# Kernel tuning notes

Hardware: AMD Instinct MI355X
Metric: run time of the kernel (lower is better)

## Reference

```python
import jax, jax.numpy as jnp
import numpy as np

D_MODEL = 1024
NUM_HEADS = 16
HEAD_DIM = D_MODEL // NUM_HEADS
HIDDEN = 4096
EPS = 1e-10


def _layernorm(x, gamma, beta):
    mean = jnp.mean(x, axis=-1, keepdims=True)
    var = jnp.var(x, axis=-1, keepdims=True)  # unbiased=False
    return gamma * (x - mean) / jnp.sqrt(var + EPS) + beta


def setup_inputs() -> dict:
    key = jax.random.key(0)
    ks = jax.random.split(key, 16)
    s = 0.02
    d, h = D_MODEL, HIDDEN
    inp = {
        "x": jax.random.normal(ks[0], (4, 2048, d), dtype=jnp.float32),
        "Wq": jax.random.normal(ks[1], (d, d), dtype=jnp.float32) * s,
        "bq": jnp.zeros((d,), jnp.float32),
        "Wk": jax.random.normal(ks[2], (d, d), dtype=jnp.float32) * s,
        "bk": jnp.zeros((d,), jnp.float32),
        "Wv": jax.random.normal(ks[3], (d, d), dtype=jnp.float32) * s,
        "bv": jnp.zeros((d,), jnp.float32),
        "Wo": jax.random.normal(ks[4], (d, d), dtype=jnp.float32) * s,
        "bo": jnp.zeros((d,), jnp.float32),
        "W1": jax.random.normal(ks[5], (d, h), dtype=jnp.float32) * s,
        "b1": jnp.zeros((h,), jnp.float32),
        "W2": jax.random.normal(ks[6], (h, d), dtype=jnp.float32) * s,
        "b2": jnp.zeros((d,), jnp.float32),
        "gamma1": jnp.ones((d,), jnp.float32),
        "beta1": jnp.zeros((d,), jnp.float32),
        "gamma2": jnp.ones((d,), jnp.float32),
        "beta2": jnp.zeros((d,), jnp.float32),
    }
    return inp


def reference(x, Wq, bq, Wk, bk, Wv, bv, Wo, bo, W1, b1, W2, b2,
              gamma1, beta1, gamma2, beta2):
    B, S, D = x.shape
    H, hd = NUM_HEADS, HEAD_DIM
    scale = jnp.sqrt(jnp.float32(hd))

    # --- sublayer 1: self-attention on norm(x), residual add ---
    xn = _layernorm(x, gamma1, beta1)
    Q = (xn @ Wq + bq).reshape(B, S, H, hd).transpose(0, 2, 1, 3)  # [B,H,S,hd]
    K = (xn @ Wk + bk).reshape(B, S, H, hd).transpose(0, 2, 1, 3)
    V = (xn @ Wv + bv).reshape(B, S, H, hd).transpose(0, 2, 1, 3)
    scores = jnp.einsum("bhqd,bhkd->bhqk", Q, K) / scale  # [B,H,S,S]
    attn = jax.nn.softmax(scores, axis=-1)
    ctx = jnp.einsum("bhqk,bhkd->bhqd", attn, V)  # [B,H,S,hd]
    ctx = ctx.transpose(0, 2, 1, 3).reshape(B, S, D)
    x = x + (ctx @ Wo + bo)

    # --- sublayer 2: FFN on norm(x), residual add ---
    xn = _layernorm(x, gamma2, beta2)
    h = jax.nn.gelu(xn @ W1 + b1, approximate=False)  # torch F.gelu default = erf
    x = x + (h @ W2 + b2)
    return x
```

## Files before the change

kernel.cpp:

```cpp
#include <hip/hip_runtime.h>
#include <stdint.h>

#define D_MODEL 1024
#define HIDDEN  4096
#define SEQ     2048
#define NTOK    8192
#define NHEAD   16
#define HDIM    64

typedef unsigned short u16;
typedef __attribute__((ext_vector_type(8))) __bf16 bf16x8;
typedef __attribute__((ext_vector_type(4))) float f32x4;

__device__ __forceinline__ u16 f2bf(float f) {
  union { float f; unsigned u; } c; c.f = f;
  unsigned u = c.u + 0x7fffu + ((c.u >> 16) & 1u);
  return (u16)(u >> 16);
}

__device__ __forceinline__ void gload16(const void* g, void* l) {
  __builtin_amdgcn_global_load_lds((const __attribute__((address_space(1))) void*)g,
                                   (__attribute__((address_space(3))) void*)l, 16, 0, 0);
}

__global__ void transpose_cvt4(const float* __restrict__ A0, const float* __restrict__ A1,
                               const float* __restrict__ A2, const float* __restrict__ A3,
                               u16* __restrict__ O) {
  __shared__ float t[32][33];
  const int z = blockIdx.z;
  const float* W = (z == 0) ? A0 : (z == 1) ? A1 : (z == 2) ? A2 : A3;
  u16* Wt = O + ((size_t)z << 20);
  const int k0 = blockIdx.y * 32, n0 = blockIdx.x * 32;
  const int tx = threadIdx.x, ty = threadIdx.y;
#pragma unroll
  for (int p = 0; p < 4; ++p)
    t[ty + p * 8][tx] = W[(size_t)(k0 + ty + p * 8) * D_MODEL + n0 + tx];
  __syncthreads();
#pragma unroll
  for (int p = 0; p < 4; ++p) {
    const int n = ty + p * 8;
    Wt[(size_t)(n0 + n) * D_MODEL + k0 + tx] = f2bf(t[tx][n]);
  }
}

__global__ void transpose_cvt(const float* __restrict__ W, u16* __restrict__ Wt, int K, int N) {
  __shared__ float t[32][33];
  const int k0 = blockIdx.y * 32, n0 = blockIdx.x * 32;
  const int tx = threadIdx.x, ty = threadIdx.y;
#pragma unroll
  for (int p = 0; p < 4; ++p)
    t[ty + p * 8][tx] = W[(size_t)(k0 + ty + p * 8) * N + n0 + tx];
  __syncthreads();
#pragma unroll
  for (int p = 0; p < 4; ++p) {
    const int n = ty + p * 8;
    Wt[(size_t)(n0 + n) * K + k0 + tx] = f2bf(t[tx][n]);
  }
}

__global__ __launch_bounds__(256)
void ln_kernel(const float* __restrict__ x, const float* __restrict__ gamma,
               const float* __restrict__ beta, u16* __restrict__ out) {
  const int row = blockIdx.x;
  const int tid = threadIdx.x;
  const float4 v = ((const float4*)(x + (size_t)row * D_MODEL))[tid];
  float s = v.x + v.y + v.z + v.w;
  float q = v.x * v.x + v.y * v.y + v.z * v.z + v.w * v.w;
#pragma unroll
  for (int o = 32; o > 0; o >>= 1) { s += __shfl_down(s, o); q += __shfl_down(q, o); }
  __shared__ float ps[4], pq[4];
  const int wid = tid >> 6, lane = tid & 63;
  if (lane == 0) { ps[wid] = s; pq[wid] = q; }
  __syncthreads();
  s = ps[0] + ps[1] + ps[2] + ps[3];
  q = pq[0] + pq[1] + pq[2] + pq[3];
  const float mean = s * (1.0f / D_MODEL);
  const float var = q * (1.0f / D_MODEL) - mean * mean;
  const float rstd = rsqrtf(var + 1e-10f);
  const float4 gv = ((const float4*)gamma)[tid];
  const float4 bv = ((const float4*)beta)[tid];
  ushort4 o4;
  o4.x = f2bf((v.x - mean) * rstd * gv.x + bv.x);
  o4.y = f2bf((v.y - mean) * rstd * gv.y + bv.y);
  o4.z = f2bf((v.z - mean) * rstd * gv.z + bv.z);
  o4.w = f2bf((v.w - mean) * rstd * gv.w + bv.w);
  ((ushort4*)(out + (size_t)row * D_MODEL))[tid] = o4;
}

template <int EPI, int KPY, int KPX>
__global__ __launch_bounds__(256, 3)
void gemm64(const u16* __restrict__ A, const u16* __restrict__ Bt,
            const float* __restrict__ bias, const float* __restrict__ bias2,
            const float* __restrict__ res, void* __restrict__ outp, void* __restrict__ outp2,
            int M, int N, int K) {
  __shared__ u16 As[128 * 64];
  __shared__ u16 Bs[128 * 64];
  const int tid = threadIdx.x;
  const int wid = tid >> 6, lane = tid & 63;
  const int g = lane >> 4, lr = lane & 15;
  const int wm = (wid & 1) << 6, wn = (wid >> 1) << 6;

  const int xcd = blockIdx.x & 7, l = blockIdx.x >> 3;
  int bx, by;
  if (KPY > 0) { by = xcd * KPY + (l % KPY); bx = l / KPY; }
  else         { bx = xcd * KPX + (l % KPX); by = l / KPX; }
  const int m0 = by * 128, n0 = bx * 128;

  const int NT = K >> 6;

  const int r0 = tid >> 3;
  const int csw = ((tid & 7) ^ (r0 & 7)) << 3;
  const u16* pA[4];
  const u16* pB[4];
#pragma unroll
  for (int i = 0; i < 4; ++i) {
    pA[i] = A + (size_t)(m0 + r0 + i * 32) * K + csw;
    pB[i] = Bt + (size_t)(n0 + r0 + i * 32) * K + csw;
  }
  const int db = (tid & 192) * 16;

  f32x4 acc[4][4] = {};

  for (int t = 0; t < NT; ++t) {
    __syncthreads();
#pragma unroll
    for (int i = 0; i < 4; ++i) {
      gload16(pA[i], (char*)As + db + i * 4096);
      gload16(pB[i], (char*)Bs + db + i * 4096);
      pA[i] += 64; pB[i] += 64;
    }
    __syncthreads();

#pragma unroll
    for (int ks = 0; ks < 2; ++ks) {
      bf16x8 af[4], bfr[4];
#pragma unroll
      for (int f = 0; f < 4; ++f) {
        const int ra = wm + f * 16 + lr;
        const int rb = wn + f * 16 + lr;
        const int co = ((ks * 4 + g) ^ (lr & 7)) * 8;
        af[f] = *(const bf16x8*)(As + ra * 64 + co);
        bfr[f] = *(const bf16x8*)(Bs + rb * 64 + co);
      }
      __builtin_amdgcn_s_setprio(1);
#pragma unroll
      for (int mf = 0; mf < 4; ++mf)
#pragma unroll
        for (int nf = 0; nf < 4; ++nf)
          acc[mf][nf] =
              __builtin_amdgcn_mfma_f32_16x16x32_bf16(af[mf], bfr[nf], acc[mf][nf], 0, 0, 0);
      __builtin_amdgcn_s_setprio(0);
    }
  }

#pragma unroll
  for (int mf = 0; mf < 4; ++mf)
#pragma unroll
    for (int nf = 0; nf < 4; ++nf) {
      const int gn = n0 + wn + nf * 16 + lr;
      const int gm = m0 + wm + mf * 16 + 4 * g;
#pragma unroll
      for (int r = 0; r < 4; ++r) {
        const float av = acc[mf][nf][r];
        if (EPI == 0) {
          ((u16*)outp)[(size_t)(gm + r) * N + gn] = f2bf(av + bias[gn]);
        } else if (EPI == 1) {
          const size_t idx = (size_t)(gm + r) * N + gn;
          ((float*)outp)[idx] = av + bias[gn] + res[idx];
        } else if (EPI == 2) {
          const float v = av + bias[gn];
          ((u16*)outp)[(size_t)(gm + r) * N + gn] =
              f2bf(0.5f * v * (1.0f + erff(v * 0.7071067811865475f)));
        } else if (EPI == 3) {
          const int gn_p = (gn & ~63) | ((gn & 15) << 2) | ((gn >> 4) & 3);
          ((u16*)outp)[(size_t)(gm + r) * N + gn_p] = f2bf(av + bias[gm + r]);
        } else {
          const int side = gn >> 10, col = gn & 1023;
          u16* o = (u16*)(side ? outp2 : outp);
          float t_ = av + (side ? bias2[col] : bias[col]);
          if (!side) t_ *= 0.18033688011112042f;
          o[(size_t)(gm + r) * 1024 + col] = f2bf(t_);
        }
      }
    }
}

__global__ __launch_bounds__(256, 4)
void attn_kernel(const u16* __restrict__ Q, const u16* __restrict__ K,
                 const u16* __restrict__ Vt, u16* __restrict__ ctxo) {
  const int L = blockIdx.x;
  const int q0 = ((L >> 3) & 15) * 128;
  const int bh = ((L >> 7) << 3) | (L & 7);
  const int b = bh >> 4, h = bh & 15;
  const int tid = threadIdx.x, wid = tid >> 6, lane = tid & 63;
  const int g = lane >> 4, lr = lane & 15;
  const size_t base = ((size_t)b * SEQ) * D_MODEL + h * HDIM;
  const size_t vbase = ((size_t)h * HDIM) * NTOK + (size_t)b * SEQ;

#define AST 76
  __shared__ u16 Ks[64 * AST];
  __shared__ u16 Vts[64 * AST];
  __shared__ u16 Ps[128 * AST];

  const int qw = wid * 32;

#pragma unroll
  for (int i = 0; i < 4; ++i) {
    const int ch = tid + 256 * i, row = ch >> 3, j = ch & 7;
    *(bf16x8*)(Ps + row * AST + j * 8) =
        *(const bf16x8*)(Q + base + (size_t)(q0 + row) * D_MODEL + j * 8);
  }
  __syncthreads();
  bf16x8 aq[2][2];
#pragma unroll
  for (int qf = 0; qf < 2; ++qf)
#pragma unroll
    for (int ks = 0; ks < 2; ++ks)
      aq[qf][ks] = *(const bf16x8*)(Ps + (qw + qf * 16 + lr) * AST + ks * 32 + g * 8);

  f32x4 o[2][4] = {};
  float lrun[2][4] = {};

  for (int kv0 = 0; kv0 < SEQ; kv0 += 64) {
    __syncthreads();
#pragma unroll
    for (int i = 0; i < 2; ++i) {
      const int row = (tid >> 3) + i * 32, j = tid & 7;
      *(bf16x8*)(Ks + row * AST + j * 8) =
          *(const bf16x8*)(K + base + (size_t)(kv0 + row) * D_MODEL + j * 8);
      *(bf16x8*)(Vts + row * AST + j * 8) =
          *(const bf16x8*)(Vt + vbase + (size_t)row * NTOK + kv0 + j * 8);
    }
    __syncthreads();

    f32x4 s[2][4] = {};
    __builtin_amdgcn_s_setprio(1);
#pragma unroll
    for (int ks = 0; ks < 2; ++ks)
#pragma unroll
      for (int kf = 0; kf < 4; ++kf) {
        const bf16x8 bk = *(const bf16x8*)(Ks + (kf * 16 + lr) * AST + ks * 32 + g * 8);
#pragma unroll
        for (int qf = 0; qf < 2; ++qf)
          s[qf][kf] = __builtin_amdgcn_mfma_f32_16x16x32_bf16(aq[qf][ks], bk, s[qf][kf], 0, 0, 0);
      }
    __builtin_amdgcn_s_setprio(0);

#pragma unroll
    for (int qf = 0; qf < 2; ++qf)
#pragma unroll
      for (int r = 0; r < 4; ++r) {
        float p0, p1, p2, p3;
        asm("v_exp_f32 %0, %1" : "=v"(p0) : "v"(s[qf][0][r]));
        asm("v_exp_f32 %0, %1" : "=v"(p1) : "v"(s[qf][1][r]));
        asm("v_exp_f32 %0, %1" : "=v"(p2) : "v"(s[qf][2][r]));
        asm("v_exp_f32 %0, %1" : "=v"(p3) : "v"(s[qf][3][r]));
        lrun[qf][r] += (p0 + p1) + (p2 + p3);
        unsigned lo, hi;
        asm("v_cvt_pk_bf16_f32 %0, %1, %2" : "=v"(lo) : "v"(p0), "v"(p1));
        asm("v_cvt_pk_bf16_f32 %0, %1, %2" : "=v"(hi) : "v"(p2), "v"(p3));
        *(uint2*)(Ps + (qw + qf * 16 + 4 * g + r) * AST + lr * 4) = make_uint2(lo, hi);
      }
    asm volatile("s_waitcnt lgkmcnt(0)" ::: "memory");

    __builtin_amdgcn_s_setprio(1);
#pragma unroll
    for (int ks = 0; ks < 2; ++ks) {
      bf16x8 pf[2];
#pragma unroll
      for (int qf = 0; qf < 2; ++qf)
        pf[qf] = *(const bf16x8*)(Ps + (qw + qf * 16 + lr) * AST + ks * 32 + g * 8);
#pragma unroll
      for (int df = 0; df < 4; ++df) {
        const bf16x8 vf = *(const bf16x8*)(Vts + (df * 16 + lr) * AST + ks * 32 + g * 8);
#pragma unroll
        for (int qf = 0; qf < 2; ++qf)
          o[qf][df] = __builtin_amdgcn_mfma_f32_16x16x32_bf16(pf[qf], vf, o[qf][df], 0, 0, 0);
      }
    }
    __builtin_amdgcn_s_setprio(0);
  }

#pragma unroll
  for (int off = 1; off < 16; off <<= 1)
#pragma unroll
    for (int qf = 0; qf < 2; ++qf)
#pragma unroll
      for (int r = 0; r < 4; ++r)
        lrun[qf][r] += __shfl_xor(lrun[qf][r], off);

#pragma unroll
  for (int qf = 0; qf < 2; ++qf)
#pragma unroll
    for (int r = 0; r < 4; ++r) {
      const float rinv = 1.0f / lrun[qf][r];
      const int qrow = q0 + qw + qf * 16 + 4 * g + r;
#pragma unroll
      for (int df = 0; df < 4; ++df)
        ctxo[base + (size_t)qrow * D_MODEL + df * 16 + lr] = f2bf(o[qf][df][r] * rinv);
    }
#undef AST
}

extern "C" void kernel_launch(void* const* d_in, const int* in_sizes, int n_in,
                              void* d_out, int out_size, void* d_ws, size_t ws_size,
                              hipStream_t stream) {
  const float* x  = (const float*)d_in[0];
  const float* Wq = (const float*)d_in[1];
  const float* bq = (const float*)d_in[2];
  const float* Wk = (const float*)d_in[3];
  const float* bk = (const float*)d_in[4];
  const float* Wv = (const float*)d_in[5];
  const float* bv = (const float*)d_in[6];
  const float* Wo = (const float*)d_in[7];
  const float* bo = (const float*)d_in[8];
  const float* W1 = (const float*)d_in[9];
  const float* b1 = (const float*)d_in[10];
  const float* W2 = (const float*)d_in[11];
  const float* b2 = (const float*)d_in[12];
  const float* gamma1 = (const float*)d_in[13];
  const float* beta1  = (const float*)d_in[14];
  const float* gamma2 = (const float*)d_in[15];
  const float* beta2  = (const float*)d_in[16];
  float* out = (float*)d_out;

  const size_t M1 = 1u << 20;
  u16* w   = (u16*)d_ws;
  u16* WtQ = w;
  u16* WtV = w + 2 * M1;
  u16* WtO = w + 3 * M1;
  u16* Wt1 = w + 4 * M1;
  u16* Wt2 = w + 8 * M1;
  u16* xn  = w + 12 * M1;
  u16* Qb  = w + 20 * M1;
  u16* Kb  = w + 28 * M1;
  u16* Vtb = w + 36 * M1;
  u16* ctx = w + 44 * M1;
  u16* hb  = w + 20 * M1;
  float* x1 = (float*)(w + 52 * M1);

  const dim3 tb(32, 8);
  transpose_cvt4<<<dim3(32, 32, 4), tb, 0, stream>>>(Wq, Wk, Wv, Wo, WtQ);
  transpose_cvt<<<dim3(HIDDEN / 32, D_MODEL / 32), tb, 0, stream>>>(W1, Wt1, D_MODEL, HIDDEN);
  transpose_cvt<<<dim3(D_MODEL / 32, HIDDEN / 32), tb, 0, stream>>>(W2, Wt2, HIDDEN, D_MODEL);

  ln_kernel<<<NTOK, 256, 0, stream>>>(x, gamma1, beta1, xn);

  gemm64<6, 8, 0><<<1024, 256, 0, stream>>>(xn, WtQ, bq, bk, nullptr, Qb, Kb,
                                            NTOK, 2048, D_MODEL);
  gemm64<3, 0, 8><<<512, 256, 0, stream>>>(WtV, xn, bv, nullptr, nullptr, Vtb, nullptr,
                                           D_MODEL, NTOK, D_MODEL);

  attn_kernel<<<1024, 256, 0, stream>>>(Qb, Kb, Vtb, ctx);

  gemm64<1, 8, 0><<<512, 256, 0, stream>>>(ctx, WtO, bo, nullptr, x, x1, nullptr,
                                           NTOK, D_MODEL, D_MODEL);

  ln_kernel<<<NTOK, 256, 0, stream>>>(x1, gamma2, beta2, xn);

  gemm64<2, 8, 0><<<2048, 256, 0, stream>>>(xn, Wt1, b1, nullptr, nullptr, hb, nullptr,
                                            NTOK, HIDDEN, D_MODEL);
  gemm64<1, 8, 0><<<512, 256, 0, stream>>>(hb, Wt2, b2, nullptr, x1, out, nullptr,
                                           NTOK, D_MODEL, HIDDEN);
}
```

Measured before the change: 353.3 us.

## Add 256x256 ping-pong pipelined GEMM kernel for FFN up-projection

Adds a new GEMM kernel with 256x256 output tiles, 512 threads and double-buffered LDS. It overlaps global-to-LDS loads with MFMA work through explicit vmcnt and barrier scheduling and raises MFMA priority with s_setprio. Only the FFN up-projection (W1 with GELU epilogue) uses it, replacing the smaller-tile gemm64. The goal is more operand reuse and better latency hiding, at the cost of one block per CU and heavy register and LDS use.

Result: slower. 366.0 us (+3.6%).

```diff
diff --git a/kernel.cpp b/kernel.cpp
--- a/kernel.cpp
+++ b/kernel.cpp
@@ -185,6 +185,138 @@
     }
 }
 
+template <int MH, int NH>
+__device__ __forceinline__ void mmq(f32x4 (&acc)[8][4], const bf16x8 (&av)[4][2],
+                                    const bf16x8 (&bv)[2][2]) {
+  __builtin_amdgcn_s_setprio(1);
+#pragma unroll
+  for (int f = 0; f < 4; ++f)
+#pragma unroll
+    for (int n = 0; n < 2; ++n)
+#pragma unroll
+      for (int ks = 0; ks < 2; ++ks)
+        acc[MH * 4 + f][NH * 2 + n] = __builtin_amdgcn_mfma_f32_16x16x32_bf16(
+            av[f][ks], bv[n][ks], acc[MH * 4 + f][NH * 2 + n], 0, 0, 0);
+  __builtin_amdgcn_s_setprio(0);
+}
+
+template <int EPI, int KPY, int KPX>
+__global__ __launch_bounds__(512, 1)
+void gemm256p(const u16* __restrict__ A, const u16* __restrict__ Bt,
+              const float* __restrict__ bias, const float* __restrict__ res,
+              void* __restrict__ outp, int M, int N, int K) {
+  __shared__ u16 Ls[65536];
+  const int tid = threadIdx.x;
+  const int wid = tid >> 6, lane = tid & 63;
+  const int g = lane >> 4, lr = lane & 15;
+  const int wm = wid >> 2, wn = wid & 3;
+
+  const int xcd = blockIdx.x & 7, l = blockIdx.x >> 3;
+  int bx, by;
+  if (KPY > 0) { by = xcd * KPY + (l % KPY); bx = l / KPY; }
+  else         { bx = xcd * KPX + (l % KPX); by = l / KPX; }
+  const int m0 = by * 256, n0 = bx * 256;
+
+  const int NT = K >> 6;
+
+  const int r0 = tid >> 3;
+  const int cc0 = ((tid & 7) ^ (r0 & 7)) << 3;
+  const u16* Abase = A + (size_t)(m0 + r0) * K + cc0;
+  const u16* Bbase = Bt + (size_t)(n0 + r0) * K + cc0;
+  const int dstb = wid << 10;
+
+  auto sA = [&](int d, int h, int tk) {
+    const u16* p = Abase + (size_t)(h * 128) * K + tk * 64;
+    char* q_ = (char*)Ls + d * 65536 + h * 16384 + dstb;
+    gload16(p, q_);
+    gload16(p + (size_t)64 * K, q_ + 8192);
+  };
+  auto sB = [&](int d, int h, int tk) {
+    const u16* p = Bbase + (size_t)(h * 128) * K + tk * 64;
+    char* q_ = (char*)Ls + d * 65536 + 32768 + h * 16384 + dstb;
+    gload16(p, q_);
+    gload16(p + (size_t)64 * K, q_ + 8192);
+  };
+
+  const int cof0 = ((g) ^ (lr & 7)) << 3;
+  const int cof1 = ((4 | g) ^ (lr & 7)) << 3;
+  const int aB = wm * 8192 + lr * 64;
+  const int bB = 16384 + (wn >> 1) * 8192 + (wn & 1) * 4096 + lr * 64;
+
+  f32x4 acc[8][4] = {};
+  bf16x8 a[4][2], a2[4][2], b[2][2], b2[2][2];
+
+  auto rdA = [&](bf16x8 (&dst)[4][2], int D, int mh) {
+#pragma unroll
+    for (int f = 0; f < 4; ++f) {
+      dst[f][0] = *(const bf16x8*)(Ls + D + aB + (mh * 4 + f) * 1024 + cof0);
+      dst[f][1] = *(const bf16x8*)(Ls + D + aB + (mh * 4 + f) * 1024 + cof1);
+    }
+  };
+  auto rdB = [&](bf16x8 (&dst)[2][2], int D, int nh) {
+#pragma unroll
+    for (int f = 0; f < 2; ++f) {
+      dst[f][0] = *(const bf16x8*)(Ls + D + bB + (nh * 2 + f) * 1024 + cof0);
+      dst[f][1] = *(const bf16x8*)(Ls + D + bB + (nh * 2 + f) * 1024 + cof1);
+    }
+  };
+
+#define BAR asm volatile("s_barrier" ::: "memory")
+#define LG0 asm volatile("s_waitcnt lgkmcnt(0)" ::: "memory")
+#define VM6 asm volatile("s_waitcnt vmcnt(6)" ::: "memory")
+#define VM0 asm volatile("s_waitcnt vmcnt(0)" ::: "memory")
+
+  sA(0, 0, 0); sA(0, 1, 0); sB(0, 0, 0); sB(0, 1, 0);
+  sA(1, 0, 1); sA(1, 1, 1); sB(1, 0, 1);
+  VM6;
+  BAR;
+
+  for (int T = 0; T < NT; T += 2) {
+    const bool s2 = (T + 2) < NT;
+    rdA(a, 0, 0); rdB(b, 0, 0); sB(1, 1, T + 1);
+    BAR; LG0; mmq<0, 0>(acc, a, b); BAR;
+    rdA(a2, 0, 1);
+    BAR; LG0; mmq<1, 0>(acc, a2, b); BAR;
+    rdB(b2, 0, 1); if (s2) sA(0, 0, T + 2);
+    BAR; LG0; mmq<1, 1>(acc, a2, b2); BAR;
+    if (s2) { sA(0, 1, T + 2); sB(0, 0, T + 2); VM6; } else VM0;
+    BAR; mmq<0, 1>(acc, a, b2); BAR;
+    rdA(a, 32768, 0); rdB(b, 32768, 0); if (s2) sB(0, 1, T + 2);
+    BAR; LG0; mmq<0, 0>(acc, a, b); BAR;
+    rdA(a2, 32768, 1);
+    BAR; LG0; mmq<1, 0>(acc, a2, b); BAR;
+    rdB(b2, 32768, 1); if (s2) sA(1, 0, T + 3);
+    BAR; LG0; mmq<1, 1>(acc, a2, b2); BAR;
+    if (s2) { sA(1, 1, T + 3); sB(1, 0, T + 3); VM6; } else VM0;
+    BAR; mmq<0, 1>(acc, a, b2); BAR;
+  }
+#undef BAR
+#undef LG0
+#undef VM6
+#undef VM0
+
+#pragma unroll
+  for (int mf = 0; mf < 8; ++mf)
+#pragma unroll
+    for (int nf = 0; nf < 4; ++nf) {
+      const int gn = n0 + wn * 64 + nf * 16 + lr;
+      const int gm = m0 + wm * 128 + mf * 16 + 4 * g;
+      const float bb = bias[gn];
+#pragma unroll
+      for (int r = 0; r < 4; ++r) {
+        const float av = acc[mf][nf][r];
+        if (EPI == 1) {
+          const size_t idx = (size_t)(gm + r) * N + gn;
+          ((float*)outp)[idx] = av + bb + res[idx];
+        } else {
+          const float v = av + bb;
+          ((u16*)outp)[(size_t)(gm + r) * N + gn] =
+              f2bf(0.5f * v * (1.0f + erff(v * 0.7071067811865475f)));
+        }
+      }
+    }
+}
+
 __global__ __launch_bounds__(256, 4)
 void attn_kernel(const u16* __restrict__ Q, const u16* __restrict__ K,
                  const u16* __restrict__ Vt, u16* __restrict__ ctxo) {
@@ -358,8 +490,8 @@
 
   ln_kernel<<<NTOK, 256, 0, stream>>>(x1, gamma2, beta2, xn);
 
-  gemm64<2, 8, 0><<<2048, 256, 0, stream>>>(xn, Wt1, b1, nullptr, nullptr, hb, nullptr,
-                                            NTOK, HIDDEN, D_MODEL);
+  gemm256p<2, 4, 0><<<512, 512, 0, stream>>>(xn, Wt1, b1, nullptr, hb,
+                                             NTOK, HIDDEN, D_MODEL);
   gemm64<1, 8, 0><<<512, 256, 0, stream>>>(hb, Wt2, b2, nullptr, x1, out, nullptr,
                                            NTOK, D_MODEL, HIDDEN);
 }
```
